# Optimization experiments

Hardware: AMD Instinct MI355X
Metric: run time of the kernel (lower is better)

Reference implementation:

```python
import jax, jax.numpy as jnp
import numpy as np

NUM_HEADS_Q = 32
NUM_HEADS_KV = 8
HEAD_DIM = 128
GROUPS = NUM_HEADS_Q // NUM_HEADS_KV


def rotate_half(x):
    d = x.shape[-1] // 2
    return jnp.concatenate([-x[..., d:], x[..., :d]], axis=-1)


def apply_rope(x, freq):
    # x: (b, h, s, d); freq: (1, 1, s, d) angles, broadcast over heads
    return x * jnp.cos(freq) + rotate_half(x) * jnp.sin(freq)


def setup_inputs() -> dict:
    key = jax.random.key(0)
    ks = jax.random.split(key, 6)
    b, s, d = 1, 2048, 4096
    x = jax.random.normal(ks[0], (b, s, d), dtype=jnp.float32)
    freq = jax.random.uniform(ks[1], (1, 1, s, HEAD_DIM), dtype=jnp.float32)
    sc = 1.0 / np.sqrt(d)
    wq = jax.random.normal(ks[2], (NUM_HEADS_Q * HEAD_DIM, d), dtype=jnp.float32) * sc
    wk = jax.random.normal(ks[3], (NUM_HEADS_KV * HEAD_DIM, d), dtype=jnp.float32) * sc
    wv = jax.random.normal(ks[4], (NUM_HEADS_KV * HEAD_DIM, d), dtype=jnp.float32) * sc
    wo = jax.random.normal(ks[5], (d, NUM_HEADS_Q * HEAD_DIM), dtype=jnp.float32) * sc
    return {"x": x, "freq": freq, "wq": wq, "wk": wk, "wv": wv, "wo": wo}


def reference(x, freq, wq, wk, wv, wo):
    b, s, d = x.shape
    # projections (nn.Linear: x @ W.T)
    q = (x @ wq.T).reshape(b, s, NUM_HEADS_Q, HEAD_DIM).transpose(0, 2, 1, 3)
    k = (x @ wk.T).reshape(b, s, NUM_HEADS_KV, HEAD_DIM).transpose(0, 2, 1, 3)
    v = (x @ wv.T).reshape(b, s, NUM_HEADS_KV, HEAD_DIM).transpose(0, 2, 1, 3)
    # past_kv is None -> seq_len offset 0
    q = apply_rope(q, freq)
    k = apply_rope(k, freq)
    k_new, v_new = k, v
    # repeat_interleave kv heads to match q heads (GQA)
    kr = jnp.repeat(k, GROUPS, axis=1)
    vr = jnp.repeat(v, GROUPS, axis=1)
    # scores: (b, hq, s, s)
    scores = jnp.einsum('bhqd,bhkd->bhqk', q, kr)
    causal = jnp.tril(jnp.ones((s, s), dtype=bool))
    scores = jnp.where(causal, scores, -jnp.inf)
    weights = jax.nn.softmax(scores * (HEAD_DIM ** -0.5), axis=-1)
    out = jnp.einsum('bhqk,bhkd->bhqd', weights, vr)
    out = out.transpose(0, 2, 1, 3).reshape(b, s, NUM_HEADS_Q * HEAD_DIM)
    return out @ wo.T, k_new, v_new
```

## Files before the change

kernel.cpp:

```cpp
#include <hip/hip_runtime.h>
#include <math.h>

#define S_LEN 2048
#define DMODEL 4096
#define NHQ 32
#define NHKV 8
#define HD 128
#define DQ 4096
#define DKV 1024

typedef __attribute__((ext_vector_type(8))) short bf16x8;
typedef __attribute__((ext_vector_type(4))) float f32x4;
typedef __attribute__((ext_vector_type(8))) unsigned short u16x8;

__device__ __forceinline__ unsigned short f2bf(float f) {
    unsigned u = __builtin_bit_cast(unsigned, f);
    u += 0x7fffu + ((u >> 16) & 1u);
    return (unsigned short)(u >> 16);
}

__device__ __forceinline__ void gload16(const void* g, void* l) {
    __builtin_amdgcn_global_load_lds(
        (const __attribute__((address_space(1))) unsigned int*)g,
        (__attribute__((address_space(3))) unsigned int*)l, 16, 0, 0);
}

__global__ __launch_bounds__(256) void cvt_bf16(const float* __restrict__ src,
                                                unsigned short* __restrict__ dst, int n8)
{
    for (int i = blockIdx.x * 256 + threadIdx.x; i < n8; i += gridDim.x * 256) {
        const float4 a = ((const float4*)src)[2 * i];
        const float4 b = ((const float4*)src)[2 * i + 1];
        u16x8 o;
        o[0] = f2bf(a.x); o[1] = f2bf(a.y); o[2] = f2bf(a.z); o[3] = f2bf(a.w);
        o[4] = f2bf(b.x); o[5] = f2bf(b.y); o[6] = f2bf(b.z); o[7] = f2bf(b.w);
        ((u16x8*)dst)[i] = o;
    }
}

#define BBM 128
#define BBN 128
#define BBK 32

__global__ __launch_bounds__(256) void gemm_bf16(const unsigned short* __restrict__ A,
                                                 const unsigned short* __restrict__ B,
                                                 float* __restrict__ C,
                                                 int M, int N, int K)
{
    __shared__ __align__(16) unsigned short As[BBM * BBK];
    __shared__ __align__(16) unsigned short Bs[BBN * BBK];

    const int tid  = threadIdx.x;
    const int lane = tid & 63;
    const int w    = tid >> 6;
    const int wy   = w >> 1, wx = w & 1;
    const int bm = blockIdx.y * BBM, bn = blockIdx.x * BBN;
    const int l15 = lane & 15;
    const int lk16 = (lane >> 4) * 16;
    const int ldsWaveBase = (tid & 192) * 16;

    f32x4 acc[4][4];
    #pragma unroll
    for (int m = 0; m < 4; ++m)
        #pragma unroll
        for (int n = 0; n < 4; ++n) acc[m][n] = (f32x4){0.f, 0.f, 0.f, 0.f};

    const char* Ab = (const char*)A;
    const char* Bb = (const char*)B;
    char* AsB = (char*)As;
    char* BsB = (char*)Bs;

    for (int k0 = 0; k0 < K; k0 += BBK) {
        __syncthreads();
        #pragma unroll
        for (int c = 0; c < 2; ++c) {
            const int i = tid + c * 256;
            const int r = i >> 2;
            const int co = (i & 3) << 4;
            gload16(Ab + ((size_t)(bm + r) * K + k0) * 2 + co, AsB + ldsWaveBase + c * 4096);
            gload16(Bb + ((size_t)(bn + r) * K + k0) * 2 + co, BsB + ldsWaveBase + c * 4096);
        }
        __syncthreads();

        bf16x8 af[4], bfr[4];
        #pragma unroll
        for (int m = 0; m < 4; ++m)
            af[m] = *(const bf16x8*)(AsB + (wy * 64 + m * 16 + l15) * 64 + lk16);
        #pragma unroll
        for (int n = 0; n < 4; ++n)
            bfr[n] = *(const bf16x8*)(BsB + (wx * 64 + n * 16 + l15) * 64 + lk16);
        #pragma unroll
        for (int m = 0; m < 4; ++m)
            #pragma unroll
            for (int n = 0; n < 4; ++n)
                acc[m][n] = __builtin_amdgcn_mfma_f32_16x16x32_bf16(af[m], bfr[n], acc[m][n], 0, 0, 0);
    }

    const int rg = (lane >> 4) * 4;
    #pragma unroll
    for (int m = 0; m < 4; ++m)
        #pragma unroll
        for (int n = 0; n < 4; ++n) {
            float* Cp = C + (size_t)(bm + wy * 64 + m * 16 + rg) * N + bn + wx * 64 + n * 16 + l15;
            #pragma unroll
            for (int r = 0; r < 4; ++r) Cp[(size_t)r * N] = acc[m][n][r];
        }
}

__global__ __launch_bounds__(256) void rope_q(const float* __restrict__ q,
                                              const float* __restrict__ freq,
                                              unsigned short* __restrict__ qbf)
{
    const int idx = blockIdx.x * 256 + threadIdx.x;
    const int d = idx & 63;
    const int s = (idx >> 6) & (S_LEN - 1);
    const int h = idx >> 17;
    const float f0 = freq[s * HD + d];
    const float f1 = freq[s * HD + d + 64];
    const float x0 = q[(size_t)s * DQ + h * HD + d];
    const float x1 = q[(size_t)s * DQ + h * HD + d + 64];
    const size_t ob = ((size_t)h * S_LEN + s) * HD + d;
    qbf[ob]      = f2bf(x0 * cosf(f0) - x1 * sinf(f0));
    qbf[ob + 64] = f2bf(x1 * cosf(f1) + x0 * sinf(f1));
}

__global__ __launch_bounds__(256) void rope_kv(const float* __restrict__ kv,
                                               const float* __restrict__ freq,
                                               float* __restrict__ knew,
                                               float* __restrict__ vnew,
                                               unsigned short* __restrict__ kbf)
{
    const int idx = blockIdx.x * 256 + threadIdx.x;
    const int d = idx & 63;
    const int s = (idx >> 6) & (S_LEN - 1);
    const int h = idx >> 17;
    const float f0 = freq[s * HD + d];
    const float f1 = freq[s * HD + d + 64];
    const size_t ib = (size_t)s * 2048 + h * HD + d;
    const float k0 = kv[ib], k1 = kv[ib + 64];
    const float v0 = kv[ib + 1024], v1 = kv[ib + 1024 + 64];
    const float k0r = k0 * cosf(f0) - k1 * sinf(f0);
    const float k1r = k1 * cosf(f1) + k0 * sinf(f1);
    const size_t ob = ((size_t)h * S_LEN + s) * HD + d;
    knew[ob] = k0r;       knew[ob + 64] = k1r;
    vnew[ob] = v0;        vnew[ob + 64] = v1;
    kbf[ob]  = f2bf(k0r); kbf[ob + 64]  = f2bf(k1r);
}

__global__ __launch_bounds__(256) void transp_v(const float* __restrict__ kv,
                                                unsigned short* __restrict__ vT)
{
    __shared__ unsigned short T[64][72];
    const int s0 = blockIdx.x * 64;
    const int dt = blockIdx.y & 1;
    const int h  = blockIdx.y >> 1;
    const int d0 = dt * 64;
    const int tid = threadIdx.x;
    #pragma unroll
    for (int c = 0; c < 4; ++c) {
        const int i = tid + c * 256;
        const int r  = i >> 4;
        const int cc = (i & 15) * 4;
        const float4 v = *(const float4*)(kv + (size_t)(s0 + r) * 2048 + 1024 + h * HD + d0 + cc);
        T[r][cc + 0] = f2bf(v.x); T[r][cc + 1] = f2bf(v.y);
        T[r][cc + 2] = f2bf(v.z); T[r][cc + 3] = f2bf(v.w);
    }
    __syncthreads();
    #pragma unroll
    for (int c = 0; c < 2; ++c) {
        const int i = tid + c * 256;
        const int dr = i >> 3;
        const int sc = (i & 7) * 8;
        u16x8 o;
        #pragma unroll
        for (int j = 0; j < 8; ++j) o[j] = T[sc + j][dr];
        *(u16x8*)(vT + ((size_t)(h * HD + d0 + dr)) * S_LEN + s0 + sc) = o;
    }
}

__global__ __launch_bounds__(256) void flash_bf16(const unsigned short* __restrict__ Qbf,
                                                  const unsigned short* __restrict__ Kbf,
                                                  const unsigned short* __restrict__ VbfT,
                                                  unsigned short* __restrict__ Obf)
{
    __shared__ __align__(16) unsigned short Qs[64 * 128];
    __shared__ __align__(16) unsigned short Ks[64 * 128];
    __shared__ __align__(16) unsigned short Vs[128 * 64];
    __shared__ __align__(16) unsigned short Ps[4][16 * 64];

    const int h  = blockIdx.x;
    const int qt = blockIdx.y;
    const int hkv = h >> 2;
    const int tid = threadIdx.x;
    const int lane = tid & 63;
    const int w = tid >> 6;
    const int l15 = lane & 15;
    const int l4  = lane >> 4;
    const int ldsWaveBase = (tid & 192) * 16;

    const char* Qg = (const char*)Qbf + ((size_t)h * S_LEN + (size_t)qt * 64) * HD * 2;
    const char* Kg = (const char*)Kbf + (size_t)hkv * S_LEN * HD * 2;
    const char* Vg = (const char*)VbfT + (size_t)hkv * HD * S_LEN * 2;

    #pragma unroll
    for (int c = 0; c < 4; ++c) {
        const int i = tid + c * 256;
        const int qr = i >> 4;
        const int cc = (i & 15) ^ (qr & 7);
        gload16(Qg + (size_t)qr * 256 + cc * 16, (char*)Qs + ldsWaveBase + c * 4096);
    }

    f32x4 accO[8];
    #pragma unroll
    for (int n = 0; n < 8; ++n) accO[n] = (f32x4){0.f, 0.f, 0.f, 0.f};
    float m_i[4] = {-3e38f, -3e38f, -3e38f, -3e38f};
    float l_i[4] = {0.f, 0.f, 0.f, 0.f};
    const float qscale = 0.08838834764831845f;

    for (int kt = 0; kt <= qt; ++kt) {
        __syncthreads();
        #pragma unroll
        for (int c = 0; c < 4; ++c) {
            const int i = tid + c * 256;
            const int kr = i >> 4;
            const int cc = (i & 15) ^ (kr & 7);
            gload16(Kg + (size_t)(kt * 64 + kr) * 256 + cc * 16, (char*)Ks + ldsWaveBase + c * 4096);
        }
        #pragma unroll
        for (int c = 0; c < 4; ++c) {
            const int i = tid + c * 256;
            const int dr = i >> 3;
            const int cc = (i & 7) ^ (dr & 7);
            gload16(Vg + (size_t)dr * (S_LEN * 2) + (size_t)kt * 128 + cc * 16,
                    (char*)Vs + ldsWaveBase + c * 4096);
        }
        __syncthreads();

        f32x4 sacc[4];
        #pragma unroll
        for (int n = 0; n < 4; ++n) sacc[n] = (f32x4){0.f, 0.f, 0.f, 0.f};
        const int qrow = w * 16;
        #pragma unroll
        for (int kb = 0; kb < 4; ++kb) {
            const int arow = qrow + l15;
            const bf16x8 aq = *(const bf16x8*)((const char*)Qs + arow * 256 +
                                 ((kb * 64 + l4 * 16) ^ ((arow & 7) << 4)));
            #pragma unroll
            for (int n = 0; n < 4; ++n) {
                const int krow = n * 16 + l15;
                const bf16x8 bk = *(const bf16x8*)((const char*)Ks + krow * 256 +
                                     ((kb * 64 + l4 * 16) ^ ((krow & 7) << 4)));
                sacc[n] = __builtin_amdgcn_mfma_f32_16x16x32_bf16(aq, bk, sacc[n], 0, 0, 0);
            }
        }

        unsigned short* Pw = &Ps[w][0];
        float csc[4];
        #pragma unroll
        for (int reg = 0; reg < 4; ++reg) {
            const int qglob = qt * 64 + qrow + l4 * 4 + reg;
            float s0 = sacc[0][reg] * qscale;
            float s1 = sacc[1][reg] * qscale;
            float s2 = sacc[2][reg] * qscale;
            float s3 = sacc[3][reg] * qscale;
            if (kt == qt) {
                const int kvb = kt * 64 + l15;
                if (kvb +  0 > qglob) s0 = -3e38f;
                if (kvb + 16 > qglob) s1 = -3e38f;
                if (kvb + 32 > qglob) s2 = -3e38f;
                if (kvb + 48 > qglob) s3 = -3e38f;
            }
            float rmax = fmaxf(fmaxf(s0, s1), fmaxf(s2, s3));
            rmax = fmaxf(rmax, __shfl_xor(rmax, 1));
            rmax = fmaxf(rmax, __shfl_xor(rmax, 2));
            rmax = fmaxf(rmax, __shfl_xor(rmax, 4));
            rmax = fmaxf(rmax, __shfl_xor(rmax, 8));
            const float mnew = fmaxf(m_i[reg], rmax);
            csc[reg] = __expf(m_i[reg] - mnew);
            m_i[reg] = mnew;
            const float p0 = __expf(s0 - mnew);
            const float p1 = __expf(s1 - mnew);
            const float p2 = __expf(s2 - mnew);
            const float p3 = __expf(s3 - mnew);
            const int rl = l4 * 4 + reg;
            const int sf = (rl & 7) << 4;
            *(unsigned short*)((char*)Pw + rl * 128 + (( 0 + l15 * 2) ^ sf)) = f2bf(p0);
            *(unsigned short*)((char*)Pw + rl * 128 + ((32 + l15 * 2) ^ sf)) = f2bf(p1);
            *(unsigned short*)((char*)Pw + rl * 128 + ((64 + l15 * 2) ^ sf)) = f2bf(p2);
            *(unsigned short*)((char*)Pw + rl * 128 + ((96 + l15 * 2) ^ sf)) = f2bf(p3);
            float rsum = p0 + p1 + p2 + p3;
            rsum += __shfl_xor(rsum, 1);
            rsum += __shfl_xor(rsum, 2);
            rsum += __shfl_xor(rsum, 4);
            rsum += __shfl_xor(rsum, 8);
            l_i[reg] = l_i[reg] * csc[reg] + rsum;
        }
        #pragma unroll
        for (int n = 0; n < 8; ++n) {
            accO[n][0] *= csc[0]; accO[n][1] *= csc[1];
            accO[n][2] *= csc[2]; accO[n][3] *= csc[3];
        }

        const char* Pwb = (const char*)Pw;
        #pragma unroll
        for (int kb = 0; kb < 2; ++kb) {
            const int prow = l15;
            const bf16x8 pa = *(const bf16x8*)(Pwb + prow * 128 +
                                 ((kb * 64 + l4 * 16) ^ ((prow & 7) << 4)));
            #pragma unroll
            for (int n = 0; n < 8; ++n) {
                const int vrow = n * 16 + l15;
                const bf16x8 vb = *(const bf16x8*)((const char*)Vs + vrow * 128 +
                                     ((kb * 64 + l4 * 16) ^ ((vrow & 7) << 4)));
                accO[n] = __builtin_amdgcn_mfma_f32_16x16x32_bf16(pa, vb, accO[n], 0, 0, 0);
            }
        }
    }

    float invl[4];
    #pragma unroll
    for (int reg = 0; reg < 4; ++reg) invl[reg] = 1.f / l_i[reg];
    #pragma unroll
    for (int n = 0; n < 8; ++n)
        #pragma unroll
        for (int reg = 0; reg < 4; ++reg) {
            const int row = qt * 64 + w * 16 + l4 * 4 + reg;
            Obf[(size_t)row * DQ + h * HD + n * 16 + l15] = f2bf(accO[n][reg] * invl[reg]);
        }
}

extern "C" void kernel_launch(void* const* d_in, const int* in_sizes, int n_in,
                              void* d_out, int out_size, void* d_ws, size_t ws_size,
                              hipStream_t stream)
{
    const float* x    = (const float*)d_in[0];
    const float* freq = (const float*)d_in[1];
    const float* wq   = (const float*)d_in[2];
    const float* wk   = (const float*)d_in[3];
    const float* wv   = (const float*)d_in[4];
    const float* wo   = (const float*)d_in[5];

    float* out  = (float*)d_out;
    float* knew = out + (size_t)S_LEN * DQ;
    float* vnew = knew + (size_t)NHKV * S_LEN * HD;

    char* ws = (char*)d_ws;
    unsigned short* x_bf   = (unsigned short*)(ws);
    unsigned short* wq_bf  = (unsigned short*)(ws + (16u << 20));
    unsigned short* wkv_bf = (unsigned short*)(ws + (48u << 20));
    float*          q_f32  = (float*)(ws + (64u << 20));
    unsigned short* attn_bf= (unsigned short*)(ws + (64u << 20));
    float*          kvtmp  = (float*)(ws + (96u << 20));
    unsigned short* q_bf   = (unsigned short*)(ws + (112u << 20));
    unsigned short* k_bf   = (unsigned short*)(ws + (128u << 20));
    unsigned short* vT_bf  = (unsigned short*)(ws + (132u << 20));

    const dim3 blk(256);

    cvt_bf16<<<2048, blk, 0, stream>>>(x,  x_bf,   S_LEN * DMODEL / 8);
    cvt_bf16<<<2048, blk, 0, stream>>>(wq, wq_bf,  DQ * DMODEL / 8);
    cvt_bf16<<<2048, blk, 0, stream>>>(wk, wkv_bf, DKV * DMODEL / 8);
    cvt_bf16<<<2048, blk, 0, stream>>>(wv, wkv_bf + (size_t)DKV * DMODEL, DKV * DMODEL / 8);

    gemm_bf16<<<dim3(DQ / BBN, S_LEN / BBM), blk, 0, stream>>>(x_bf, wq_bf, q_f32, S_LEN, DQ, DMODEL);

    cvt_bf16<<<2048, blk, 0, stream>>>(wo, wq_bf, DMODEL * DQ / 8);

    gemm_bf16<<<dim3(2048 / BBN, S_LEN / BBM), blk, 0, stream>>>(x_bf, wkv_bf, kvtmp, S_LEN, 2048, DMODEL);

    rope_q<<<NHQ * S_LEN * 64 / 256, blk, 0, stream>>>(q_f32, freq, q_bf);
    rope_kv<<<NHKV * S_LEN * 64 / 256, blk, 0, stream>>>(kvtmp, freq, knew, vnew, k_bf);
    transp_v<<<dim3(S_LEN / 64, 2 * NHKV), blk, 0, stream>>>(kvtmp, vT_bf);

    flash_bf16<<<dim3(NHQ, S_LEN / 64), blk, 0, stream>>>(q_bf, k_bf, vT_bf, attn_bf);

    gemm_bf16<<<dim3(DMODEL / BBN, S_LEN / BBM), blk, 0, stream>>>(attn_bf, wq_bf, out, S_LEN, DMODEL, DMODEL);
}
```

Before: 663.0 us.

## Fuse QKV projection GEMM and double-buffer flash attention with lazy rescaling

Merges the Q and KV projection GEMMs into one N=6144 GEMM, which removes a launch and improves occupancy. Q is pre-scaled by softmax scale times log2e so the attention kernel can use exp2f. The flash kernel now keeps Q fragments in registers, double-buffers K/V tiles in LDS so the next tile loads while the current one computes, and balances causal work by interleaving short and long query tiles across blocks. It only rescales the online softmax when the row max grows by more than a threshold, and raises wave priority around the MFMA sections. The lazy rescale lets unnormalized values grow up to 2^8 before correction, which changes numerics slightly.

Result: faster. 589.4 us (-11.1%).

```diff
diff --git a/kernel.cpp b/kernel.cpp
--- a/kernel.cpp
+++ b/kernel.cpp
@@ -8,6 +8,7 @@
 #define HD 128
 #define DQ 4096
 #define DKV 1024
+#define NQKV 6144
 
 typedef __attribute__((ext_vector_type(8))) short bf16x8;
 typedef __attribute__((ext_vector_type(4))) float f32x4;
@@ -107,7 +108,9 @@
         }
 }
 
-__global__ __launch_bounds__(256) void rope_q(const float* __restrict__ q,
+#define QSC (0.08838834764831845f * 1.4426950408889634f)
+
+__global__ __launch_bounds__(256) void rope_q(const float* __restrict__ qkv,
                                               const float* __restrict__ freq,
                                               unsigned short* __restrict__ qbf)
 {
@@ -117,14 +120,14 @@
     const int h = idx >> 17;
     const float f0 = freq[s * HD + d];
     const float f1 = freq[s * HD + d + 64];
-    const float x0 = q[(size_t)s * DQ + h * HD + d];
-    const float x1 = q[(size_t)s * DQ + h * HD + d + 64];
+    const float x0 = qkv[(size_t)s * NQKV + h * HD + d];
+    const float x1 = qkv[(size_t)s * NQKV + h * HD + d + 64];
     const size_t ob = ((size_t)h * S_LEN + s) * HD + d;
-    qbf[ob]      = f2bf(x0 * cosf(f0) - x1 * sinf(f0));
-    qbf[ob + 64] = f2bf(x1 * cosf(f1) + x0 * sinf(f1));
-}
-
-__global__ __launch_bounds__(256) void rope_kv(const float* __restrict__ kv,
+    qbf[ob]      = f2bf((x0 * cosf(f0) - x1 * sinf(f0)) * QSC);
+    qbf[ob + 64] = f2bf((x1 * cosf(f1) + x0 * sinf(f1)) * QSC);
+}
+
+__global__ __launch_bounds__(256) void rope_kv(const float* __restrict__ qkv,
                                                const float* __restrict__ freq,
                                                float* __restrict__ knew,
                                                float* __restrict__ vnew,
@@ -136,9 +139,9 @@
     const int h = idx >> 17;
     const float f0 = freq[s * HD + d];
     const float f1 = freq[s * HD + d + 64];
-    const size_t ib = (size_t)s * 2048 + h * HD + d;
-    const float k0 = kv[ib], k1 = kv[ib + 64];
-    const float v0 = kv[ib + 1024], v1 = kv[ib + 1024 + 64];
+    const size_t ib = (size_t)s * NQKV + 4096 + h * HD + d;
+    const float k0 = qkv[ib], k1 = qkv[ib + 64];
+    const float v0 = qkv[ib + 1024], v1 = qkv[ib + 1024 + 64];
     const float k0r = k0 * cosf(f0) - k1 * sinf(f0);
     const float k1r = k1 * cosf(f1) + k0 * sinf(f1);
     const size_t ob = ((size_t)h * S_LEN + s) * HD + d;
@@ -147,7 +150,7 @@
     kbf[ob]  = f2bf(k0r); kbf[ob + 64]  = f2bf(k1r);
 }
 
-__global__ __launch_bounds__(256) void transp_v(const float* __restrict__ kv,
+__global__ __launch_bounds__(256) void transp_v(const float* __restrict__ qkv,
                                                 unsigned short* __restrict__ vT)
 {
     __shared__ unsigned short T[64][72];
@@ -161,7 +164,7 @@
         const int i = tid + c * 256;
         const int r  = i >> 4;
         const int cc = (i & 15) * 4;
-        const float4 v = *(const float4*)(kv + (size_t)(s0 + r) * 2048 + 1024 + h * HD + d0 + cc);
+        const float4 v = *(const float4*)(qkv + (size_t)(s0 + r) * NQKV + 5120 + h * HD + d0 + cc);
         T[r][cc + 0] = f2bf(v.x); T[r][cc + 1] = f2bf(v.y);
         T[r][cc + 2] = f2bf(v.z); T[r][cc + 3] = f2bf(v.w);
     }
@@ -183,13 +186,13 @@
                                                   const unsigned short* __restrict__ VbfT,
                                                   unsigned short* __restrict__ Obf)
 {
-    __shared__ __align__(16) unsigned short Qs[64 * 128];
-    __shared__ __align__(16) unsigned short Ks[64 * 128];
-    __shared__ __align__(16) unsigned short Vs[128 * 64];
+    __shared__ __align__(16) unsigned short Ks[2][64 * 128];
+    __shared__ __align__(16) unsigned short Vs[2][128 * 64];
     __shared__ __align__(16) unsigned short Ps[4][16 * 64];
 
     const int h  = blockIdx.x;
-    const int qt = blockIdx.y;
+    const int yq = blockIdx.y;
+    const int qt = (yq & 1) ? (31 - (yq >> 1)) : (yq >> 1);
     const int hkv = h >> 2;
     const int tid = threadIdx.x;
     const int lane = tid & 63;
@@ -198,33 +201,25 @@
     const int l4  = lane >> 4;
     const int ldsWaveBase = (tid & 192) * 16;
 
-    const char* Qg = (const char*)Qbf + ((size_t)h * S_LEN + (size_t)qt * 64) * HD * 2;
     const char* Kg = (const char*)Kbf + (size_t)hkv * S_LEN * HD * 2;
     const char* Vg = (const char*)VbfT + (size_t)hkv * HD * S_LEN * 2;
 
-    #pragma unroll
-    for (int c = 0; c < 4; ++c) {
-        const int i = tid + c * 256;
-        const int qr = i >> 4;
-        const int cc = (i & 15) ^ (qr & 7);
-        gload16(Qg + (size_t)qr * 256 + cc * 16, (char*)Qs + ldsWaveBase + c * 4096);
-    }
-
-    f32x4 accO[8];
-    #pragma unroll
-    for (int n = 0; n < 8; ++n) accO[n] = (f32x4){0.f, 0.f, 0.f, 0.f};
-    float m_i[4] = {-3e38f, -3e38f, -3e38f, -3e38f};
-    float l_i[4] = {0.f, 0.f, 0.f, 0.f};
-    const float qscale = 0.08838834764831845f;
-
-    for (int kt = 0; kt <= qt; ++kt) {
-        __syncthreads();
+    bf16x8 qf[4];
+    {
+        const char* Qg = (const char*)Qbf + ((size_t)h * S_LEN + qt * 64 + w * 16 + l15) * 256;
+        #pragma unroll
+        for (int kb = 0; kb < 4; ++kb)
+            qf[kb] = *(const bf16x8*)(Qg + kb * 64 + l4 * 16);
+    }
+
+    auto STAGE = [&](int buf, int kt) {
         #pragma unroll
         for (int c = 0; c < 4; ++c) {
             const int i = tid + c * 256;
             const int kr = i >> 4;
             const int cc = (i & 15) ^ (kr & 7);
-            gload16(Kg + (size_t)(kt * 64 + kr) * 256 + cc * 16, (char*)Ks + ldsWaveBase + c * 4096);
+            gload16(Kg + (size_t)(kt * 64 + kr) * 256 + cc * 16,
+                    (char*)Ks[buf] + ldsWaveBase + c * 4096);
         }
         #pragma unroll
         for (int c = 0; c < 4; ++c) {
@@ -232,38 +227,46 @@
             const int dr = i >> 3;
             const int cc = (i & 7) ^ (dr & 7);
             gload16(Vg + (size_t)dr * (S_LEN * 2) + (size_t)kt * 128 + cc * 16,
-                    (char*)Vs + ldsWaveBase + c * 4096);
-        }
-        __syncthreads();
+                    (char*)Vs[buf] + ldsWaveBase + c * 4096);
+        }
+    };
+
+    f32x4 accO[8];
+    #pragma unroll
+    for (int n = 0; n < 8; ++n) accO[n] = (f32x4){0.f, 0.f, 0.f, 0.f};
+    float m_i[4] = {-3e38f, -3e38f, -3e38f, -3e38f};
+    float l_i[4] = {0.f, 0.f, 0.f, 0.f};
+
+    STAGE(0, 0);
+    __syncthreads();
+
+    for (int kt = 0; kt <= qt; ++kt) {
+        const int cbuf = kt & 1;
+        if (kt < qt) STAGE(cbuf ^ 1, kt + 1);
 
         f32x4 sacc[4];
         #pragma unroll
         for (int n = 0; n < 4; ++n) sacc[n] = (f32x4){0.f, 0.f, 0.f, 0.f};
-        const int qrow = w * 16;
+        __builtin_amdgcn_s_setprio(1);
         #pragma unroll
         for (int kb = 0; kb < 4; ++kb) {
-            const int arow = qrow + l15;
-            const bf16x8 aq = *(const bf16x8*)((const char*)Qs + arow * 256 +
-                                 ((kb * 64 + l4 * 16) ^ ((arow & 7) << 4)));
             #pragma unroll
             for (int n = 0; n < 4; ++n) {
                 const int krow = n * 16 + l15;
-                const bf16x8 bk = *(const bf16x8*)((const char*)Ks + krow * 256 +
+                const bf16x8 bk = *(const bf16x8*)((const char*)Ks[cbuf] + krow * 256 +
                                      ((kb * 64 + l4 * 16) ^ ((krow & 7) << 4)));
-                sacc[n] = __builtin_amdgcn_mfma_f32_16x16x32_bf16(aq, bk, sacc[n], 0, 0, 0);
+                sacc[n] = __builtin_amdgcn_mfma_f32_16x16x32_bf16(qf[kb], bk, sacc[n], 0, 0, 0);
             }
         }
-
-        unsigned short* Pw = &Ps[w][0];
-        float csc[4];
+        __builtin_amdgcn_s_setprio(0);
+
+        float s0v[4], s1v[4], s2v[4], s3v[4], pm[4];
         #pragma unroll
         for (int reg = 0; reg < 4; ++reg) {
-            const int qglob = qt * 64 + qrow + l4 * 4 + reg;
-            float s0 = sacc[0][reg] * qscale;
-            float s1 = sacc[1][reg] * qscale;
-            float s2 = sacc[2][reg] * qscale;
-            float s3 = sacc[3][reg] * qscale;
+            float s0 = sacc[0][reg], s1 = sacc[1][reg];
+            float s2 = sacc[2][reg], s3 = sacc[3][reg];
             if (kt == qt) {
+                const int qglob = qt * 64 + w * 16 + l4 * 4 + reg;
                 const int kvb = kt * 64 + l15;
                 if (kvb +  0 > qglob) s0 = -3e38f;
                 if (kvb + 16 > qglob) s1 = -3e38f;
@@ -275,13 +278,31 @@
             rmax = fmaxf(rmax, __shfl_xor(rmax, 2));
             rmax = fmaxf(rmax, __shfl_xor(rmax, 4));
             rmax = fmaxf(rmax, __shfl_xor(rmax, 8));
-            const float mnew = fmaxf(m_i[reg], rmax);
-            csc[reg] = __expf(m_i[reg] - mnew);
-            m_i[reg] = mnew;
-            const float p0 = __expf(s0 - mnew);
-            const float p1 = __expf(s1 - mnew);
-            const float p2 = __expf(s2 - mnew);
-            const float p3 = __expf(s3 - mnew);
+            pm[reg] = rmax;
+            s0v[reg] = s0; s1v[reg] = s1; s2v[reg] = s2; s3v[reg] = s3;
+        }
+
+        const bool grew = (pm[0] > m_i[0] + 8.f) || (pm[1] > m_i[1] + 8.f) ||
+                          (pm[2] > m_i[2] + 8.f) || (pm[3] > m_i[3] + 8.f);
+        if (__any(grew)) {
+            #pragma unroll
+            for (int reg = 0; reg < 4; ++reg) {
+                const float mnew = fmaxf(m_i[reg], pm[reg]);
+                const float csc = exp2f(m_i[reg] - mnew);
+                l_i[reg] *= csc;
+                m_i[reg] = mnew;
+                #pragma unroll
+                for (int n = 0; n < 8; ++n) accO[n][reg] *= csc;
+            }
+        }
+
+        unsigned short* Pw = &Ps[w][0];
+        #pragma unroll
+        for (int reg = 0; reg < 4; ++reg) {
+            const float p0 = exp2f(s0v[reg] - m_i[reg]);
+            const float p1 = exp2f(s1v[reg] - m_i[reg]);
+            const float p2 = exp2f(s2v[reg] - m_i[reg]);
+            const float p3 = exp2f(s3v[reg] - m_i[reg]);
             const int rl = l4 * 4 + reg;
             const int sf = (rl & 7) << 4;
             *(unsigned short*)((char*)Pw + rl * 128 + (( 0 + l15 * 2) ^ sf)) = f2bf(p0);
@@ -293,28 +314,26 @@
             rsum += __shfl_xor(rsum, 2);
             rsum += __shfl_xor(rsum, 4);
             rsum += __shfl_xor(rsum, 8);
-            l_i[reg] = l_i[reg] * csc[reg] + rsum;
-        }
-        #pragma unroll
-        for (int n = 0; n < 8; ++n) {
-            accO[n][0] *= csc[0]; accO[n][1] *= csc[1];
-            accO[n][2] *= csc[2]; accO[n][3] *= csc[3];
+            l_i[reg] += rsum;
         }
 
         const char* Pwb = (const char*)Pw;
+        __builtin_amdgcn_s_setprio(1);
         #pragma unroll
         for (int kb = 0; kb < 2; ++kb) {
-            const int prow = l15;
-            const bf16x8 pa = *(const bf16x8*)(Pwb + prow * 128 +
-                                 ((kb * 64 + l4 * 16) ^ ((prow & 7) << 4)));
+            const bf16x8 pa = *(const bf16x8*)(Pwb + l15 * 128 +
+                                 ((kb * 64 + l4 * 16) ^ ((l15 & 7) << 4)));
             #pragma unroll
             for (int n = 0; n < 8; ++n) {
                 const int vrow = n * 16 + l15;
-                const bf16x8 vb = *(const bf16x8*)((const char*)Vs + vrow * 128 +
+                const bf16x8 vb = *(const bf16x8*)((const char*)Vs[cbuf] + vrow * 128 +
                                      ((kb * 64 + l4 * 16) ^ ((vrow & 7) << 4)));
                 accO[n] = __builtin_amdgcn_mfma_f32_16x16x32_bf16(pa, vb, accO[n], 0, 0, 0);
             }
         }
+        __builtin_amdgcn_s_setprio(0);
+
+        __syncthreads();
     }
 
     float invl[4];
@@ -345,34 +364,31 @@
     float* vnew = knew + (size_t)NHKV * S_LEN * HD;
 
     char* ws = (char*)d_ws;
-    unsigned short* x_bf   = (unsigned short*)(ws);
-    unsigned short* wq_bf  = (unsigned short*)(ws + (16u << 20));
-    unsigned short* wkv_bf = (unsigned short*)(ws + (48u << 20));
-    float*          q_f32  = (float*)(ws + (64u << 20));
-    unsigned short* attn_bf= (unsigned short*)(ws + (64u << 20));
-    float*          kvtmp  = (float*)(ws + (96u << 20));
-    unsigned short* q_bf   = (unsigned short*)(ws + (112u << 20));
-    unsigned short* k_bf   = (unsigned short*)(ws + (128u << 20));
-    unsigned short* vT_bf  = (unsigned short*)(ws + (132u << 20));
+    unsigned short* x_bf    = (unsigned short*)(ws);
+    unsigned short* attn_bf = (unsigned short*)(ws);
+    unsigned short* wqkv_bf = (unsigned short*)(ws + (16u << 20));
+    unsigned short* wo_bf   = (unsigned short*)(ws + (16u << 20));
+    float*          qkv_f32 = (float*)(ws + (64u << 20));
+    unsigned short* q_bf    = (unsigned short*)(ws + (112u << 20));
+    unsigned short* k_bf    = (unsigned short*)(ws + (128u << 20));
+    unsigned short* vT_bf   = (unsigned short*)(ws + (132u << 20));
 
     const dim3 blk(256);
 
-    cvt_bf16<<<2048, blk, 0, stream>>>(x,  x_bf,   S_LEN * DMODEL / 8);
-    cvt_bf16<<<2048, blk, 0, stream>>>(wq, wq_bf,  DQ * DMODEL / 8);
-    cvt_bf16<<<2048, blk, 0, stream>>>(wk, wkv_bf, DKV * DMODEL / 8);
-    cvt_bf16<<<2048, blk, 0, stream>>>(wv, wkv_bf + (size_t)DKV * DMODEL, DKV * DMODEL / 8);
-
-    gemm_bf16<<<dim3(DQ / BBN, S_LEN / BBM), blk, 0, stream>>>(x_bf, wq_bf, q_f32, S_LEN, DQ, DMODEL);
-
-    cvt_bf16<<<2048, blk, 0, stream>>>(wo, wq_bf, DMODEL * DQ / 8);
-
-    gemm_bf16<<<dim3(2048 / BBN, S_LEN / BBM), blk, 0, stream>>>(x_bf, wkv_bf, kvtmp, S_LEN, 2048, DMODEL);
-
-    rope_q<<<NHQ * S_LEN * 64 / 256, blk, 0, stream>>>(q_f32, freq, q_bf);
-    rope_kv<<<NHKV * S_LEN * 64 / 256, blk, 0, stream>>>(kvtmp, freq, knew, vnew, k_bf);
-    transp_v<<<dim3(S_LEN / 64, 2 * NHKV), blk, 0, stream>>>(kvtmp, vT_bf);
+    cvt_bf16<<<2048, blk, 0, stream>>>(x,  x_bf, S_LEN * DMODEL / 8);
+    cvt_bf16<<<2048, blk, 0, stream>>>(wq, wqkv_bf, DQ * DMODEL / 8);
+    cvt_bf16<<<1024, blk, 0, stream>>>(wk, wqkv_bf + (size_t)DQ * DMODEL, DKV * DMODEL / 8);
+    cvt_bf16<<<1024, blk, 0, stream>>>(wv, wqkv_bf + (size_t)(DQ + DKV) * DMODEL, DKV * DMODEL / 8);
+
+    gemm_bf16<<<dim3(NQKV / BBN, S_LEN / BBM), blk, 0, stream>>>(x_bf, wqkv_bf, qkv_f32, S_LEN, NQKV, DMODEL);
+
+    cvt_bf16<<<2048, blk, 0, stream>>>(wo, wo_bf, DMODEL * DQ / 8);
+
+    rope_q<<<NHQ * S_LEN * 64 / 256, blk, 0, stream>>>(qkv_f32, freq, q_bf);
+    rope_kv<<<NHKV * S_LEN * 64 / 256, blk, 0, stream>>>(qkv_f32, freq, knew, vnew, k_bf);
+    transp_v<<<dim3(S_LEN / 64, 2 * NHKV), blk, 0, stream>>>(qkv_f32, vT_bf);
 
     flash_bf16<<<dim3(NHQ, S_LEN / 64), blk, 0, stream>>>(q_bf, k_bf, vT_bf, attn_bf);
 
-    gemm_bf16<<<dim3(DMODEL / BBN, S_LEN / BBM), blk, 0, stream>>>(attn_bf, wq_bf, out, S_LEN, DMODEL, DMODEL);
-}
+    gemm_bf16<<<dim3(DMODEL / BBN, S_LEN / BBM), blk, 0, stream>>>(attn_bf, wo_bf, out, S_LEN, DMODEL, DMODEL);
+}
```
